# Kernel tuning notes

Measured on AMD Instinct MI355X. Metric: run time of the kernel, lower is better.

## Reference

```python
import jax, jax.numpy as jnp
import numpy as np

VOCAB, EMB, HID = 100000, 300, 600
B, S, N = 256, 64, 64
MAX_LEVEL = 3  # depth of the fixed 4-ary tree


def _tree():
    parent = np.zeros(N, np.int32)
    level = np.zeros(N, np.int32)
    for i in range(1, N):
        parent[i] = (i - 1) // 4
        level[i] = level[parent[i]] + 1
    return parent, level


def setup_inputs() -> dict:
    key = jax.random.key(0)
    ks = jax.random.split(key, 16)
    parent, level = _tree()
    E_tab = jax.random.normal(ks[0], (VOCAB, EMB), jnp.float32) * 0.1
    E_tab = E_tab.at[0].set(0.0)  # padding_idx=0
    return dict(
        premise_x=jax.random.randint(ks[1], (B, S), 0, VOCAB),
        hypothesis_x=jax.random.randint(ks[2], (B, S), 0, VOCAB),
        p_word_idx=jax.random.randint(ks[3], (B, N), -1, S),  # -1 => ones vector
        p_rel_id=jax.random.randint(ks[4], (B, N), -1, 4),    # 0..2 transformed, -1/3 identity
        h_word_idx=jax.random.randint(ks[5], (B, N), -1, S),
        h_rel_id=jax.random.randint(ks[6], (B, N), -1, 4),
        parent=jnp.asarray(parent),
        level=jnp.asarray(level),
        E_tab=E_tab,
        W_enc=jax.random.normal(ks[7], (3, EMB, EMB), jnp.float32) * 0.1,
        W0_w=jax.random.normal(ks[8], (HID, 6 * EMB), jnp.float32) * 0.1,
        W0_b=jax.random.normal(ks[9], (HID,), jnp.float32) * 0.1,
        W1_w=jax.random.normal(ks[10], (HID, HID), jnp.float32) * 0.1,
        W1_b=jax.random.normal(ks[11], (HID,), jnp.float32) * 0.1,
        W2_w=jax.random.normal(ks[12], (HID, HID), jnp.float32) * 0.1,
        W2_b=jax.random.normal(ks[13], (HID,), jnp.float32) * 0.1,
        Wout_w=jax.random.normal(ks[14], (3, HID), jnp.float32) * 0.1,
        Wout_b=jax.random.normal(ks[15], (3,), jnp.float32) * 0.1,
    )


def _encode_sg(seq, word_idx, rel_id, parent, level, W_enc):
    # Level-synchronous bottom-up evaluation of: leaf -> word,
    # internal -> relu(word * mean(rel-transformed children)).
    Bn, Nn = word_idx.shape
    Ed = seq.shape[-1]
    idx = jnp.clip(word_idx, 0, None)
    word = jnp.take_along_axis(seq, idx[:, :, None], axis=1)        # [B,N,E]
    word = jnp.where((word_idx == -1)[..., None], 1.0, word)        # word_idx==-1 => ones
    h = word
    pflat = (parent[None, :] + (jnp.arange(Bn) * Nn)[:, None]).reshape(-1)
    for l in range(MAX_LEVEL, 0, -1):
        is_child = jnp.broadcast_to(level[None, :] == l, (Bn, Nn))
        # per-relation linear W_enc[r]: h @ W.T (torch Linear, no bias)
        t_all = jnp.einsum('bne,rfe->bnrf', h, W_enc)               # [B,N,3,E]
        sel = jnp.clip(rel_id, 0, 2)[:, :, None, None]
        t = jnp.take_along_axis(t_all, sel, axis=2)[:, :, 0, :]
        t = jnp.where(((rel_id >= 0) & (rel_id <= 2))[..., None], t, h)
        contrib = jnp.where(is_child[..., None], t, 0.0).reshape(Bn * Nn, Ed)
        sums = jnp.zeros((Bn * Nn, Ed), h.dtype).at[pflat].add(contrib)
        counts = jnp.zeros((Bn * Nn,), h.dtype).at[pflat].add(
            is_child.astype(h.dtype).reshape(-1))
        mean = (sums / jnp.maximum(counts, 1.0)[:, None]).reshape(Bn, Nn, Ed)
        has_child = (counts.reshape(Bn, Nn) > 0)
        h = jnp.where(has_child[..., None], jax.nn.relu(word * mean), h)
    return h[:, 0, :]  # root representation


def reference(premise_x, hypothesis_x, p_word_idx, p_rel_id, h_word_idx, h_rel_id,
              parent, level, E_tab, W_enc, W0_w, W0_b, W1_w, W1_b, W2_w, W2_b,
              Wout_w, Wout_b):
    emb_p = E_tab[premise_x]      # [B,S,E]
    emb_h = E_tab[hypothesis_x]
    p_rep = emb_p.sum(axis=1)
    h_rep = emb_h.sum(axis=1)
    p_sg = _encode_sg(emb_p, p_word_idx, p_rel_id, parent, level, W_enc)
    h_sg = _encode_sg(emb_h, h_word_idx, h_rel_id, parent, level, W_enc)
    x = jnp.concatenate([p_rep, h_rep, p_rep - h_rep, p_rep * h_rep,
                         p_sg - h_sg, p_sg * h_sg], axis=1)  # [B,6E]
    h1 = jax.nn.relu(x @ W0_w.T + W0_b)
    h2 = jax.nn.relu(h1 @ W1_w.T + W1_b)
    h3 = jax.nn.relu(h2 @ W2_w.T + W2_b)
    return h3 @ Wout_w.T + Wout_b  # [B,3]
```

## Files before the change

### kernel.cpp

```cpp
#include <hip/hip_runtime.h>

constexpr int NB = 256;
constexpr int NS = 64;
constexpr int NN = 64;
constexpr int NE = 300;
constexpr int NH = 600;

typedef __attribute__((ext_vector_type(8))) short bf16x8;
typedef __attribute__((ext_vector_type(4))) float f32x4;

constexpr int KT0 = 57;
constexpr int KT1 = 19;
constexpr int NJT = 40;
constexpr int HP  = 640;

constexpr size_t OFF_REP = 0;
constexpr size_t SZ_REP  = (size_t)2*NB*NE;
constexpr size_t OFF_ROOT= OFF_REP + SZ_REP;
constexpr size_t OFF_WBF = OFF_ROOT + SZ_REP;
constexpr size_t SZ_WBF  = (size_t)3*20*10*64*8/2;
constexpr size_t OFF_W0S = OFF_WBF + SZ_WBF;
constexpr size_t SZ_W0S  = (size_t)KT0*NJT*64*8/2;
constexpr size_t OFF_W1S = OFF_W0S + SZ_W0S;
constexpr size_t SZ_W1S  = (size_t)KT1*NJT*64*8/2;
constexpr size_t OFF_W2S = OFF_W1S + SZ_W1S;
constexpr size_t OFF_XSW = OFF_W2S + SZ_W1S;
constexpr size_t SZ_XSW  = (size_t)KT0*16*64*8/2;
constexpr size_t OFF_H1  = OFF_XSW + SZ_XSW;
constexpr size_t SZ_H    = (size_t)NB*HP/2;
constexpr size_t OFF_H2  = OFF_H1 + SZ_H;
constexpr size_t OFF_H3  = OFF_H2 + SZ_H;

__device__ __forceinline__ ushort f2bf(float x) {
  unsigned u = __float_as_uint(x);
  unsigned r = (u + 0x7FFFu + ((u >> 16) & 1u)) >> 16;
  return (ushort)r;
}
__device__ __forceinline__ float bf2f(ushort u) {
  return __uint_as_float(((unsigned)u) << 16);
}

constexpr int NSWZ = 3*20*10*64;
constexpr int N0S  = KT0*NJT*64;
constexpr int N1S  = KT1*NJT*64;
constexpr int SETUP_ITEMS  = NSWZ + N0S + 2*N1S;
constexpr int SETUP_BLOCKS = SETUP_ITEMS/256;

__global__ __launch_bounds__(256)
void k_setup(const float* __restrict__ Wenc, const float* __restrict__ W0,
             const float* __restrict__ W1, const float* __restrict__ W2,
             ushort* __restrict__ Wbf, ushort* __restrict__ W0S,
             ushort* __restrict__ W1S, ushort* __restrict__ W2S) {
  int t = blockIdx.x*256 + threadIdx.x;
  if (t < NSWZ) {
    int lane = t & 63, rest = t >> 6;
    int ksi = rest % 10, rnt = rest / 10, nt = rnt % 20, r = rnt / 20;
    int f = nt*16 + (lane & 15), e0 = ksi*32 + (lane >> 4)*8;
    ushort v[8];
    #pragma unroll
    for (int j = 0; j < 8; j++) {
      int e = e0 + j;
      v[j] = (f < NE && e < NE) ? f2bf(Wenc[((size_t)r*NE + f)*NE + e]) : (ushort)0;
    }
    *reinterpret_cast<int4*>(&Wbf[(size_t)t*8]) = *reinterpret_cast<const int4*>(v);
    return;
  }
  t -= NSWZ;
  const float* W; ushort* D; int K;
  if (t < N0S)              { W = W0; D = W0S; K = 6*NE; }
  else { t -= N0S;
    if (t < N1S)            { W = W1; D = W1S; K = NH; }
    else { t -= N1S;          W = W2; D = W2S; K = NH; } }
  int lane = t & 63, g = t >> 6;
  int jt = g % NJT, kt = g / NJT;
  int j  = jt*16 + (lane & 15);
  int kb = kt*32 + (lane >> 4)*8;
  ushort v[8];
  #pragma unroll
  for (int i = 0; i < 8; i++) {
    int k = kb + i;
    v[i] = (j < NH && k < K) ? f2bf(W[(size_t)j*K + k]) : (ushort)0;
  }
  *reinterpret_cast<int4*>(&D[(size_t)t*8]) = *reinterpret_cast<const int4*>(v);
}

constexpr int TS = 328;

__global__ __launch_bounds__(256)
void k_tree(const int* __restrict__ px, const int* __restrict__ hx,
            const int* __restrict__ pwi, const int* __restrict__ prel,
            const int* __restrict__ hwi, const int* __restrict__ hrel,
            const float* __restrict__ Etab, const ushort* __restrict__ Wbf,
            float* __restrict__ rep, float* __restrict__ root) {
  __shared__ __align__(16) ushort hS[64*TS];
  __shared__ int xsh[64];
  __shared__ int wish[64];
  __shared__ int relsh[64];
  const int sb = blockIdx.x;
  const int s = sb >> 8, b = sb & 255;
  const int tid = threadIdx.x;

  if (tid < 64) xsh[tid] = ((s ? hx : px) + b*NS)[tid];
  else if (tid < 128) wish[tid-64] = ((s ? hwi : pwi) + b*NN)[tid-64];
  else if (tid < 192) relsh[tid-128] = ((s ? hrel : prel) + b*NN)[tid-128];
  __syncthreads();

  for (int e = tid; e < NE; e += 256) {
    float acc = 0.f;
    #pragma unroll 8
    for (int j = 0; j < NS; j++) acc += Etab[(size_t)xsh[j]*NE + e];
    rep[(size_t)sb*NE + e] = acc;
  }
  for (int flat = tid; flat < 64*75; flat += 256) {
    int n = flat / 75, c = flat % 75;
    int w = wish[n];
    float4 v;
    if (w < 0) v = float4{1.f,1.f,1.f,1.f};
    else v = *reinterpret_cast<const float4*>(&Etab[(size_t)xsh[w]*NE + c*4]);
    ushort4 o; o.x = f2bf(v.x); o.y = f2bf(v.y); o.z = f2bf(v.z); o.w = f2bf(v.w);
    *reinterpret_cast<ushort4*>(&hS[n*TS + c*4]) = o;
  }
  for (int z = tid; z < 64*10; z += 256) {
    int row = z / 10, cc = z % 10;
    *reinterpret_cast<unsigned*>(&hS[row*TS + 300 + cc*2]) = 0u;
  }
  __syncthreads();

  const int wave = tid >> 6, lane = tid & 63;
  const int mrow = lane & 15, quad = lane >> 4;

  {
    const int mb0 = 21, mb1 = 37, mb2 = 53;
    bf16x8 af[3][10];
    #pragma unroll
    for (int ks = 0; ks < 10; ks++) {
      af[0][ks] = *reinterpret_cast<const bf16x8*>(&hS[(mb0+mrow)*TS + ks*32 + quad*8]);
      af[1][ks] = *reinterpret_cast<const bf16x8*>(&hS[(mb1+mrow)*TS + ks*32 + quad*8]);
      int r2 = min(mb2+mrow, 63);
      af[2][ks] = *reinterpret_cast<const bf16x8*>(&hS[r2*TS + ks*32 + quad*8]);
    }
    __syncthreads();
    for (int pr = wave; pr < 57; pr += 4) {
      int r = pr / 19, nt = pr % 19;
      const ushort* Wb = &Wbf[(size_t)((r*20 + nt)*10)*64*8];
      f32x4 acc0 = f32x4{0.f,0.f,0.f,0.f};
      f32x4 acc1 = f32x4{0.f,0.f,0.f,0.f};
      f32x4 acc2 = f32x4{0.f,0.f,0.f,0.f};
      #pragma unroll
      for (int ks = 0; ks < 10; ks++) {
        bf16x8 bf = *reinterpret_cast<const bf16x8*>(&Wb[((size_t)ks*64 + lane)*8]);
        acc0 = __builtin_amdgcn_mfma_f32_16x16x32_bf16(af[0][ks], bf, acc0, 0, 0, 0);
        acc1 = __builtin_amdgcn_mfma_f32_16x16x32_bf16(af[1][ks], bf, acc1, 0, 0, 0);
        acc2 = __builtin_amdgcn_mfma_f32_16x16x32_bf16(af[2][ks], bf, acc2, 0, 0, 0);
      }
      int f = nt*16 + mrow;
      if (f < NE) {
        #pragma unroll
        for (int reg = 0; reg < 4; reg++) {
          int m = quad*4 + reg;
          int c0 = mb0 + m, c1 = mb1 + m, c2 = mb2 + m;
          if (relsh[c0] == r) hS[c0*TS + f] = f2bf(acc0[reg]);
          if (relsh[c1] == r) hS[c1*TS + f] = f2bf(acc1[reg]);
          if (c2 < 64 && relsh[c2] == r) hS[c2*TS + f] = f2bf(acc2[reg]);
        }
      }
    }
    __syncthreads();
    for (int f = tid; f < NE; f += 256) {
      #pragma unroll
      for (int p = 5; p <= 15; p++) {
        int nc = (p == 15) ? 3 : 4;
        float sum = 0.f;
        for (int j = 0; j < nc; j++) sum += bf2f(hS[(4*p+1+j)*TS + f]);
        float v = bf2f(hS[p*TS + f]) * sum * (1.0f/(float)nc);
        hS[p*TS + f] = f2bf(v > 0.f ? v : 0.f);
      }
    }
    __syncthreads();
  }

  {
    bf16x8 af[10];
    #pragma unroll
    for (int ks = 0; ks < 10; ks++)
      af[ks] = *reinterpret_cast<const bf16x8*>(&hS[(5+mrow)*TS + ks*32 + quad*8]);
    __syncthreads();
    for (int pr = wave; pr < 57; pr += 4) {
      int r = pr / 19, nt = pr % 19;
      const ushort* Wb = &Wbf[(size_t)((r*20 + nt)*10)*64*8];
      f32x4 acc = f32x4{0.f,0.f,0.f,0.f};
      #pragma unroll
      for (int ks = 0; ks < 10; ks++) {
        bf16x8 bf = *reinterpret_cast<const bf16x8*>(&Wb[((size_t)ks*64 + lane)*8]);
        acc = __builtin_amdgcn_mfma_f32_16x16x32_bf16(af[ks], bf, acc, 0, 0, 0);
      }
      int f = nt*16 + mrow;
      if (f < NE) {
        #pragma unroll
        for (int reg = 0; reg < 4; reg++) {
          int c = 5 + quad*4 + reg;
          if (relsh[c] == r) hS[c*TS + f] = f2bf(acc[reg]);
        }
      }
    }
    __syncthreads();
    for (int f = tid; f < NE; f += 256) {
      #pragma unroll
      for (int p = 1; p <= 4; p++) {
        float sum = 0.f;
        #pragma unroll
        for (int j = 0; j < 4; j++) sum += bf2f(hS[(4*p+1+j)*TS + f]);
        float v = bf2f(hS[p*TS + f]) * sum * 0.25f;
        hS[p*TS + f] = f2bf(v > 0.f ? v : 0.f);
      }
    }
    __syncthreads();
  }

  {
    bool rp0 = (relsh[1]==0)|(relsh[2]==0)|(relsh[3]==0)|(relsh[4]==0);
    bool rp1 = (relsh[1]==1)|(relsh[2]==1)|(relsh[3]==1)|(relsh[4]==1);
    bool rp2 = (relsh[1]==2)|(relsh[2]==2)|(relsh[3]==2)|(relsh[4]==2);
    bf16x8 af[10];
    #pragma unroll
    for (int ks = 0; ks < 10; ks++)
      af[ks] = *reinterpret_cast<const bf16x8*>(&hS[(1+min(mrow,3))*TS + ks*32 + quad*8]);
    __syncthreads();
    for (int pr = wave; pr < 57; pr += 4) {
      int r = pr / 19, nt = pr % 19;
      if ((r==0 && !rp0) || (r==1 && !rp1) || (r==2 && !rp2)) continue;
      const ushort* Wb = &Wbf[(size_t)((r*20 + nt)*10)*64*8];
      f32x4 acc = f32x4{0.f,0.f,0.f,0.f};
      #pragma unroll
      for (int ks = 0; ks < 10; ks++) {
        bf16x8 bf = *reinterpret_cast<const bf16x8*>(&Wb[((size_t)ks*64 + lane)*8]);
        acc = __builtin_amdgcn_mfma_f32_16x16x32_bf16(af[ks], bf, acc, 0, 0, 0);
      }
      int f = nt*16 + mrow;
      if (f < NE) {
        #pragma unroll
        for (int reg = 0; reg < 4; reg++) {
          int m = quad*4 + reg;
          if (m < 4 && relsh[1+m] == r) hS[(1+m)*TS + f] = f2bf(acc[reg]);
        }
      }
    }
    __syncthreads();
    for (int f = tid; f < NE; f += 256) {
      float sum = 0.f;
      #pragma unroll
      for (int c = 1; c <= 4; c++) sum += bf2f(hS[c*TS + f]);
      float v = bf2f(hS[0*TS + f]) * sum * 0.25f;
      root[(size_t)sb*NE + f] = v > 0.f ? v : 0.f;
    }
  }
}

constexpr int FEAT_ITEMS  = KT0*16*64;
constexpr int FEAT_BLOCKS = FEAT_ITEMS/256;

__global__ __launch_bounds__(256)
void k_feat(const float* __restrict__ rep, const float* __restrict__ root,
            ushort* __restrict__ Xsw) {
  int t = blockIdx.x*256 + threadIdx.x;
  int lane = t & 63, g = t >> 6;
  int mt = g % 16, kt = g / 16;
  int b  = mt*16 + (lane & 15);
  int kb = kt*32 + (lane >> 4)*8;
  const float* rp = rep  + (size_t)b*NE;
  const float* rh = rep  + (size_t)(NB+b)*NE;
  const float* tp = root + (size_t)b*NE;
  const float* th = root + (size_t)(NB+b)*NE;
  ushort v[8];
  #pragma unroll
  for (int i = 0; i < 8; i++) {
    int k = kb + i;
    float x = 0.f;
    if (k < 6*NE) {
      int seg = k / NE, e = k - seg*NE;
      switch (seg) {
        case 0:  x = rp[e]; break;
        case 1:  x = rh[e]; break;
        case 2:  x = rp[e] - rh[e]; break;
        case 3:  x = rp[e] * rh[e]; break;
        case 4:  x = tp[e] - th[e]; break;
        default: x = tp[e] * th[e]; break;
      }
    }
    v[i] = f2bf(x);
  }
  *reinterpret_cast<int4*>(&Xsw[(size_t)t*8]) = *reinterpret_cast<const int4*>(v);
}

__device__ __forceinline__ void fc_epi(f32x4 acc, int row, int j,
                                       const float* __restrict__ bias,
                                       ushort* __restrict__ hout) {
  float bj = (j < NH) ? bias[j] : 0.f;
  #pragma unroll
  for (int r = 0; r < 4; r++) {
    float v = acc[r] + bj;
    v = v > 0.f ? v : 0.f;
    if (j < 608) hout[(size_t)(row + r)*HP + j] = f2bf(v);
  }
}

__global__ __launch_bounds__(256)
void k_gemm(const ushort* __restrict__ A, const ushort* __restrict__ Wsw,
            const float* __restrict__ bias, ushort* __restrict__ hout,
            int nstep, int mode) {
  const int tid = threadIdx.x;
  const int wv = tid >> 6, lane = tid & 63;
  const int bx = blockIdx.x, by = blockIdx.y;
  const int b0 = bx*64, j0 = by*64;

  const ushort* ap;
  size_t astride;
  if (mode == 0) {
    ap = A + ((size_t)((size_t)bx*4 + wv)*64 + lane)*8;
    astride = (size_t)16*64*8;
  } else {
    ap = A + (size_t)(b0 + wv*16 + (lane & 15))*HP + (lane >> 4)*8;
    astride = 32;
  }
  const ushort* wp = Wsw + ((size_t)(by*4)*64 + lane)*8;
  constexpr size_t WSTRIDE = (size_t)NJT*64*8;

  f32x4 acc0{0.f,0.f,0.f,0.f}, acc1{0.f,0.f,0.f,0.f};
  f32x4 acc2{0.f,0.f,0.f,0.f}, acc3{0.f,0.f,0.f,0.f};
  for (int t = 0; t < nstep; t++) {
    bf16x8 a  = *reinterpret_cast<const bf16x8*>(ap);
    bf16x8 w0 = *reinterpret_cast<const bf16x8*>(wp);
    bf16x8 w1 = *reinterpret_cast<const bf16x8*>(wp + 512);
    bf16x8 w2 = *reinterpret_cast<const bf16x8*>(wp + 1024);
    bf16x8 w3 = *reinterpret_cast<const bf16x8*>(wp + 1536);
    acc0 = __builtin_amdgcn_mfma_f32_16x16x32_bf16(a, w0, acc0, 0, 0, 0);
    acc1 = __builtin_amdgcn_mfma_f32_16x16x32_bf16(a, w1, acc1, 0, 0, 0);
    acc2 = __builtin_amdgcn_mfma_f32_16x16x32_bf16(a, w2, acc2, 0, 0, 0);
    acc3 = __builtin_amdgcn_mfma_f32_16x16x32_bf16(a, w3, acc3, 0, 0, 0);
    ap += astride;
    wp += WSTRIDE;
  }
  int row = b0 + wv*16 + (lane >> 4)*4;
  int jb  = j0 + (lane & 15);
  fc_epi(acc0, row, jb +  0, bias, hout);
  fc_epi(acc1, row, jb + 16, bias, hout);
  fc_epi(acc2, row, jb + 32, bias, hout);
  fc_epi(acc3, row, jb + 48, bias, hout);
}

__global__ __launch_bounds__(64)
void k_out(const ushort* __restrict__ h3, const float* __restrict__ Wout,
           const float* __restrict__ bout, float* __restrict__ out) {
  int b = blockIdx.x, tid = threadIdx.x;
  float a0 = 0.f, a1 = 0.f, a2 = 0.f;
  for (int k = tid; k < NH; k += 64) {
    float xv = bf2f(h3[(size_t)b*HP + k]);
    a0 += xv * Wout[k];
    a1 += xv * Wout[NH + k];
    a2 += xv * Wout[2*NH + k];
  }
  #pragma unroll
  for (int off = 32; off > 0; off >>= 1) {
    a0 += __shfl_down(a0, off, 64);
    a1 += __shfl_down(a1, off, 64);
    a2 += __shfl_down(a2, off, 64);
  }
  if (tid == 0) {
    out[b*3 + 0] = a0 + bout[0];
    out[b*3 + 1] = a1 + bout[1];
    out[b*3 + 2] = a2 + bout[2];
  }
}

extern "C" void kernel_launch(void* const* d_in, const int* in_sizes, int n_in,
                              void* d_out, int out_size, void* d_ws, size_t ws_size,
                              hipStream_t stream) {
  const int*   px    = (const int*)d_in[0];
  const int*   hx    = (const int*)d_in[1];
  const int*   pwi   = (const int*)d_in[2];
  const int*   prel  = (const int*)d_in[3];
  const int*   hwi   = (const int*)d_in[4];
  const int*   hrel  = (const int*)d_in[5];
  const float* Etab  = (const float*)d_in[8];
  const float* Wenc  = (const float*)d_in[9];
  const float* W0w   = (const float*)d_in[10];
  const float* W0b   = (const float*)d_in[11];
  const float* W1w   = (const float*)d_in[12];
  const float* W1b   = (const float*)d_in[13];
  const float* W2w   = (const float*)d_in[14];
  const float* W2b   = (const float*)d_in[15];
  const float* Woutw = (const float*)d_in[16];
  const float* Woutb = (const float*)d_in[17];

  float* ws   = (float*)d_ws;
  float*  rep  = ws + OFF_REP;
  float*  root = ws + OFF_ROOT;
  ushort* Wbf  = (ushort*)(ws + OFF_WBF);
  ushort* W0S  = (ushort*)(ws + OFF_W0S);
  ushort* W1S  = (ushort*)(ws + OFF_W1S);
  ushort* W2S  = (ushort*)(ws + OFF_W2S);
  ushort* Xsw  = (ushort*)(ws + OFF_XSW);
  ushort* h1   = (ushort*)(ws + OFF_H1);
  ushort* h2   = (ushort*)(ws + OFF_H2);
  ushort* h3   = (ushort*)(ws + OFF_H3);
  float* outp = (float*)d_out;

  dim3 blk(256);
  k_setup<<<dim3(SETUP_BLOCKS), blk, 0, stream>>>(
      Wenc, W0w, W1w, W2w, Wbf, W0S, W1S, W2S);
  k_tree<<<dim3(2*NB), blk, 0, stream>>>(
      px, hx, pwi, prel, hwi, hrel, Etab, Wbf, rep, root);
  k_feat<<<dim3(FEAT_BLOCKS), blk, 0, stream>>>(rep, root, Xsw);
  k_gemm<<<dim3(4,10), blk, 0, stream>>>(Xsw, W0S, W0b, h1, KT0, 0);
  k_gemm<<<dim3(4,10), blk, 0, stream>>>(h1,  W1S, W1b, h2, KT1, 1);
  k_gemm<<<dim3(4,10), blk, 0, stream>>>(h2,  W2S, W2b, h3, KT1, 1);
  k_out<<<dim3(NB), dim3(64), 0, stream>>>(h3, Woutw, Woutb, outp);
}
```

Baseline: 314.2 us.

## Fuse all stages into one persistent kernel with grid barriers and split-K FC

Replaces the seven separate launches (weight swizzle, tree encoder, feature build, three FC GEMMs, output) with one persistent 512-block kernel synchronised by an atomic-counter grid barrier. The FC layers now use 160 blocks, with each wave taking a K-slice and partial sums reduced through shared memory, instead of 40 blocks. The aim is to remove launch gaps and raise parallelism in the small GEMMs. The risks are spin-barrier cost and a deadlock if not all blocks are co-resident.

```diff
diff --git a/kernel.cpp b/kernel.cpp
--- a/kernel.cpp
+++ b/kernel.cpp
@@ -5,6 +5,7 @@
 constexpr int NN = 64;
 constexpr int NE = 300;
 constexpr int NH = 600;
+constexpr int NBLK = 512;
 
 typedef __attribute__((ext_vector_type(8))) short bf16x8;
 typedef __attribute__((ext_vector_type(4))) float f32x4;
@@ -30,6 +31,7 @@
 constexpr size_t SZ_H    = (size_t)NB*HP/2;
 constexpr size_t OFF_H2  = OFF_H1 + SZ_H;
 constexpr size_t OFF_H3  = OFF_H2 + SZ_H;
+constexpr size_t OFF_CNT = OFF_H3 + SZ_H;
 
 __device__ __forceinline__ ushort f2bf(float x) {
   unsigned u = __float_as_uint(x);
@@ -40,294 +42,51 @@
   return __uint_as_float(((unsigned)u) << 16);
 }
 
+__device__ __forceinline__ void gridbar(unsigned* cnt, unsigned target) {
+  __syncthreads();
+  if (threadIdx.x == 0) {
+    __threadfence();
+    atomicAdd(cnt, 1u);
+    while (atomicAdd(cnt, 0u) < target) __builtin_amdgcn_s_sleep(2);
+    __threadfence();
+  }
+  __syncthreads();
+}
+
 constexpr int NSWZ = 3*20*10*64;
 constexpr int N0S  = KT0*NJT*64;
 constexpr int N1S  = KT1*NJT*64;
-constexpr int SETUP_ITEMS  = NSWZ + N0S + 2*N1S;
-constexpr int SETUP_BLOCKS = SETUP_ITEMS/256;
-
-__global__ __launch_bounds__(256)
-void k_setup(const float* __restrict__ Wenc, const float* __restrict__ W0,
-             const float* __restrict__ W1, const float* __restrict__ W2,
-             ushort* __restrict__ Wbf, ushort* __restrict__ W0S,
-             ushort* __restrict__ W1S, ushort* __restrict__ W2S) {
-  int t = blockIdx.x*256 + threadIdx.x;
-  if (t < NSWZ) {
-    int lane = t & 63, rest = t >> 6;
-    int ksi = rest % 10, rnt = rest / 10, nt = rnt % 20, r = rnt / 20;
-    int f = nt*16 + (lane & 15), e0 = ksi*32 + (lane >> 4)*8;
-    ushort v[8];
-    #pragma unroll
-    for (int j = 0; j < 8; j++) {
-      int e = e0 + j;
-      v[j] = (f < NE && e < NE) ? f2bf(Wenc[((size_t)r*NE + f)*NE + e]) : (ushort)0;
-    }
-    *reinterpret_cast<int4*>(&Wbf[(size_t)t*8]) = *reinterpret_cast<const int4*>(v);
-    return;
-  }
-  t -= NSWZ;
-  const float* W; ushort* D; int K;
-  if (t < N0S)              { W = W0; D = W0S; K = 6*NE; }
-  else { t -= N0S;
-    if (t < N1S)            { W = W1; D = W1S; K = NH; }
-    else { t -= N1S;          W = W2; D = W2S; K = NH; } }
-  int lane = t & 63, g = t >> 6;
-  int jt = g % NJT, kt = g / NJT;
-  int j  = jt*16 + (lane & 15);
-  int kb = kt*32 + (lane >> 4)*8;
-  ushort v[8];
-  #pragma unroll
-  for (int i = 0; i < 8; i++) {
-    int k = kb + i;
-    v[i] = (j < NH && k < K) ? f2bf(W[(size_t)j*K + k]) : (ushort)0;
-  }
-  *reinterpret_cast<int4*>(&D[(size_t)t*8]) = *reinterpret_cast<const int4*>(v);
-}
+constexpr int SETUP_ITEMS = NSWZ + N0S + 2*N1S;
+constexpr int FEAT_ITEMS  = KT0*16*64;
 
 constexpr int TS = 328;
 
-__global__ __launch_bounds__(256)
-void k_tree(const int* __restrict__ px, const int* __restrict__ hx,
-            const int* __restrict__ pwi, const int* __restrict__ prel,
-            const int* __restrict__ hwi, const int* __restrict__ hrel,
-            const float* __restrict__ Etab, const ushort* __restrict__ Wbf,
-            float* __restrict__ rep, float* __restrict__ root) {
-  __shared__ __align__(16) ushort hS[64*TS];
-  __shared__ int xsh[64];
-  __shared__ int wish[64];
-  __shared__ int relsh[64];
-  const int sb = blockIdx.x;
-  const int s = sb >> 8, b = sb & 255;
-  const int tid = threadIdx.x;
-
-  if (tid < 64) xsh[tid] = ((s ? hx : px) + b*NS)[tid];
-  else if (tid < 128) wish[tid-64] = ((s ? hwi : pwi) + b*NN)[tid-64];
-  else if (tid < 192) relsh[tid-128] = ((s ? hrel : prel) + b*NN)[tid-128];
-  __syncthreads();
-
-  for (int e = tid; e < NE; e += 256) {
-    float acc = 0.f;
-    #pragma unroll 8
-    for (int j = 0; j < NS; j++) acc += Etab[(size_t)xsh[j]*NE + e];
-    rep[(size_t)sb*NE + e] = acc;
-  }
-  for (int flat = tid; flat < 64*75; flat += 256) {
-    int n = flat / 75, c = flat % 75;
-    int w = wish[n];
-    float4 v;
-    if (w < 0) v = float4{1.f,1.f,1.f,1.f};
-    else v = *reinterpret_cast<const float4*>(&Etab[(size_t)xsh[w]*NE + c*4]);
-    ushort4 o; o.x = f2bf(v.x); o.y = f2bf(v.y); o.z = f2bf(v.z); o.w = f2bf(v.w);
-    *reinterpret_cast<ushort4*>(&hS[n*TS + c*4]) = o;
-  }
-  for (int z = tid; z < 64*10; z += 256) {
-    int row = z / 10, cc = z % 10;
-    *reinterpret_cast<unsigned*>(&hS[row*TS + 300 + cc*2]) = 0u;
-  }
-  __syncthreads();
-
-  const int wave = tid >> 6, lane = tid & 63;
-  const int mrow = lane & 15, quad = lane >> 4;
-
-  {
-    const int mb0 = 21, mb1 = 37, mb2 = 53;
-    bf16x8 af[3][10];
-    #pragma unroll
-    for (int ks = 0; ks < 10; ks++) {
-      af[0][ks] = *reinterpret_cast<const bf16x8*>(&hS[(mb0+mrow)*TS + ks*32 + quad*8]);
-      af[1][ks] = *reinterpret_cast<const bf16x8*>(&hS[(mb1+mrow)*TS + ks*32 + quad*8]);
-      int r2 = min(mb2+mrow, 63);
-      af[2][ks] = *reinterpret_cast<const bf16x8*>(&hS[r2*TS + ks*32 + quad*8]);
-    }
-    __syncthreads();
-    for (int pr = wave; pr < 57; pr += 4) {
-      int r = pr / 19, nt = pr % 19;
-      const ushort* Wb = &Wbf[(size_t)((r*20 + nt)*10)*64*8];
-      f32x4 acc0 = f32x4{0.f,0.f,0.f,0.f};
-      f32x4 acc1 = f32x4{0.f,0.f,0.f,0.f};
-      f32x4 acc2 = f32x4{0.f,0.f,0.f,0.f};
-      #pragma unroll
-      for (int ks = 0; ks < 10; ks++) {
-        bf16x8 bf = *reinterpret_cast<const bf16x8*>(&Wb[((size_t)ks*64 + lane)*8]);
-        acc0 = __builtin_amdgcn_mfma_f32_16x16x32_bf16(af[0][ks], bf, acc0, 0, 0, 0);
-        acc1 = __builtin_amdgcn_mfma_f32_16x16x32_bf16(af[1][ks], bf, acc1, 0, 0, 0);
-        acc2 = __builtin_amdgcn_mfma_f32_16x16x32_bf16(af[2][ks], bf, acc2, 0, 0, 0);
-      }
-      int f = nt*16 + mrow;
-      if (f < NE) {
-        #pragma unroll
-        for (int reg = 0; reg < 4; reg++) {
-          int m = quad*4 + reg;
-          int c0 = mb0 + m, c1 = mb1 + m, c2 = mb2 + m;
-          if (relsh[c0] == r) hS[c0*TS + f] = f2bf(acc0[reg]);
-          if (relsh[c1] == r) hS[c1*TS + f] = f2bf(acc1[reg]);
-          if (c2 < 64 && relsh[c2] == r) hS[c2*TS + f] = f2bf(acc2[reg]);
-        }
-      }
-    }
-    __syncthreads();
-    for (int f = tid; f < NE; f += 256) {
-      #pragma unroll
-      for (int p = 5; p <= 15; p++) {
-        int nc = (p == 15) ? 3 : 4;
-        float sum = 0.f;
-        for (int j = 0; j < nc; j++) sum += bf2f(hS[(4*p+1+j)*TS + f]);
-        float v = bf2f(hS[p*TS + f]) * sum * (1.0f/(float)nc);
-        hS[p*TS + f] = f2bf(v > 0.f ? v : 0.f);
-      }
-    }
-    __syncthreads();
-  }
-
-  {
-    bf16x8 af[10];
-    #pragma unroll
-    for (int ks = 0; ks < 10; ks++)
-      af[ks] = *reinterpret_cast<const bf16x8*>(&hS[(5+mrow)*TS + ks*32 + quad*8]);
-    __syncthreads();
-    for (int pr = wave; pr < 57; pr += 4) {
-      int r = pr / 19, nt = pr % 19;
-      const ushort* Wb = &Wbf[(size_t)((r*20 + nt)*10)*64*8];
-      f32x4 acc = f32x4{0.f,0.f,0.f,0.f};
-      #pragma unroll
-      for (int ks = 0; ks < 10; ks++) {
-        bf16x8 bf = *reinterpret_cast<const bf16x8*>(&Wb[((size_t)ks*64 + lane)*8]);
-        acc = __builtin_amdgcn_mfma_f32_16x16x32_bf16(af[ks], bf, acc, 0, 0, 0);
-      }
-      int f = nt*16 + mrow;
-      if (f < NE) {
-        #pragma unroll
-        for (int reg = 0; reg < 4; reg++) {
-          int c = 5 + quad*4 + reg;
-          if (relsh[c] == r) hS[c*TS + f] = f2bf(acc[reg]);
-        }
-      }
-    }
-    __syncthreads();
-    for (int f = tid; f < NE; f += 256) {
-      #pragma unroll
-      for (int p = 1; p <= 4; p++) {
-        float sum = 0.f;
-        #pragma unroll
-        for (int j = 0; j < 4; j++) sum += bf2f(hS[(4*p+1+j)*TS + f]);
-        float v = bf2f(hS[p*TS + f]) * sum * 0.25f;
-        hS[p*TS + f] = f2bf(v > 0.f ? v : 0.f);
-      }
-    }
-    __syncthreads();
-  }
-
-  {
-    bool rp0 = (relsh[1]==0)|(relsh[2]==0)|(relsh[3]==0)|(relsh[4]==0);
-    bool rp1 = (relsh[1]==1)|(relsh[2]==1)|(relsh[3]==1)|(relsh[4]==1);
-    bool rp2 = (relsh[1]==2)|(relsh[2]==2)|(relsh[3]==2)|(relsh[4]==2);
-    bf16x8 af[10];
-    #pragma unroll
-    for (int ks = 0; ks < 10; ks++)
-      af[ks] = *reinterpret_cast<const bf16x8*>(&hS[(1+min(mrow,3))*TS + ks*32 + quad*8]);
-    __syncthreads();
-    for (int pr = wave; pr < 57; pr += 4) {
-      int r = pr / 19, nt = pr % 19;
-      if ((r==0 && !rp0) || (r==1 && !rp1) || (r==2 && !rp2)) continue;
-      const ushort* Wb = &Wbf[(size_t)((r*20 + nt)*10)*64*8];
-      f32x4 acc = f32x4{0.f,0.f,0.f,0.f};
-      #pragma unroll
-      for (int ks = 0; ks < 10; ks++) {
-        bf16x8 bf = *reinterpret_cast<const bf16x8*>(&Wb[((size_t)ks*64 + lane)*8]);
-        acc = __builtin_amdgcn_mfma_f32_16x16x32_bf16(af[ks], bf, acc, 0, 0, 0);
-      }
-      int f = nt*16 + mrow;
-      if (f < NE) {
-        #pragma unroll
-        for (int reg = 0; reg < 4; reg++) {
-          int m = quad*4 + reg;
-          if (m < 4 && relsh[1+m] == r) hS[(1+m)*TS + f] = f2bf(acc[reg]);
-        }
-      }
-    }
-    __syncthreads();
-    for (int f = tid; f < NE; f += 256) {
-      float sum = 0.f;
-      #pragma unroll
-      for (int c = 1; c <= 4; c++) sum += bf2f(hS[c*TS + f]);
-      float v = bf2f(hS[0*TS + f]) * sum * 0.25f;
-      root[(size_t)sb*NE + f] = v > 0.f ? v : 0.f;
-    }
-  }
-}
-
-constexpr int FEAT_ITEMS  = KT0*16*64;
-constexpr int FEAT_BLOCKS = FEAT_ITEMS/256;
-
-__global__ __launch_bounds__(256)
-void k_feat(const float* __restrict__ rep, const float* __restrict__ root,
-            ushort* __restrict__ Xsw) {
-  int t = blockIdx.x*256 + threadIdx.x;
-  int lane = t & 63, g = t >> 6;
-  int mt = g % 16, kt = g / 16;
-  int b  = mt*16 + (lane & 15);
-  int kb = kt*32 + (lane >> 4)*8;
-  const float* rp = rep  + (size_t)b*NE;
-  const float* rh = rep  + (size_t)(NB+b)*NE;
-  const float* tp = root + (size_t)b*NE;
-  const float* th = root + (size_t)(NB+b)*NE;
-  ushort v[8];
-  #pragma unroll
-  for (int i = 0; i < 8; i++) {
-    int k = kb + i;
-    float x = 0.f;
-    if (k < 6*NE) {
-      int seg = k / NE, e = k - seg*NE;
-      switch (seg) {
-        case 0:  x = rp[e]; break;
-        case 1:  x = rh[e]; break;
-        case 2:  x = rp[e] - rh[e]; break;
-        case 3:  x = rp[e] * rh[e]; break;
-        case 4:  x = tp[e] - th[e]; break;
-        default: x = tp[e] * th[e]; break;
-      }
-    }
-    v[i] = f2bf(x);
-  }
-  *reinterpret_cast<int4*>(&Xsw[(size_t)t*8]) = *reinterpret_cast<const int4*>(v);
-}
-
-__device__ __forceinline__ void fc_epi(f32x4 acc, int row, int j,
-                                       const float* __restrict__ bias,
-                                       ushort* __restrict__ hout) {
-  float bj = (j < NH) ? bias[j] : 0.f;
-  #pragma unroll
-  for (int r = 0; r < 4; r++) {
-    float v = acc[r] + bj;
-    v = v > 0.f ? v : 0.f;
-    if (j < 608) hout[(size_t)(row + r)*HP + j] = f2bf(v);
-  }
-}
-
-__global__ __launch_bounds__(256)
-void k_gemm(const ushort* __restrict__ A, const ushort* __restrict__ Wsw,
-            const float* __restrict__ bias, ushort* __restrict__ hout,
-            int nstep, int mode) {
-  const int tid = threadIdx.x;
-  const int wv = tid >> 6, lane = tid & 63;
-  const int bx = blockIdx.x, by = blockIdx.y;
-  const int b0 = bx*64, j0 = by*64;
+__device__ void fc_layer(const ushort* __restrict__ Arm,
+                         const ushort* __restrict__ Xs,
+                         const ushort* __restrict__ Wsw,
+                         const float* __restrict__ bias,
+                         ushort* __restrict__ hout,
+                         int nkt, float* red) {
+  const int blk = blockIdx.x;
+  if (blk >= 160) return;
+  const int tid = threadIdx.x, wv = tid >> 6, lane = tid & 63;
+  const int bx = blk / 10, by = blk % 10;
 
   const ushort* ap;
-  size_t astride;
-  if (mode == 0) {
-    ap = A + ((size_t)((size_t)bx*4 + wv)*64 + lane)*8;
-    astride = (size_t)16*64*8;
+  size_t ast;
+  if (Xs) {
+    ap  = Xs + (((size_t)wv*16 + bx)*64 + lane)*8;
+    ast = (size_t)4*16*64*8;
   } else {
-    ap = A + (size_t)(b0 + wv*16 + (lane & 15))*HP + (lane >> 4)*8;
-    astride = 32;
-  }
-  const ushort* wp = Wsw + ((size_t)(by*4)*64 + lane)*8;
-  constexpr size_t WSTRIDE = (size_t)NJT*64*8;
+    ap  = Arm + ((size_t)(bx*16 + (lane & 15)))*HP + ((lane >> 4)*8) + (size_t)wv*32;
+    ast = (size_t)4*32;
+  }
+  const ushort* wp = Wsw + (((size_t)wv*NJT + (size_t)by*4)*64 + lane)*8;
+  const size_t wst = (size_t)4*NJT*64*8;
 
   f32x4 acc0{0.f,0.f,0.f,0.f}, acc1{0.f,0.f,0.f,0.f};
   f32x4 acc2{0.f,0.f,0.f,0.f}, acc3{0.f,0.f,0.f,0.f};
-  for (int t = 0; t < nstep; t++) {
+  for (int t = wv; t < nkt; t += 4) {
     bf16x8 a  = *reinterpret_cast<const bf16x8*>(ap);
     bf16x8 w0 = *reinterpret_cast<const bf16x8*>(wp);
     bf16x8 w1 = *reinterpret_cast<const bf16x8*>(wp + 512);
@@ -337,38 +96,312 @@
     acc1 = __builtin_amdgcn_mfma_f32_16x16x32_bf16(a, w1, acc1, 0, 0, 0);
     acc2 = __builtin_amdgcn_mfma_f32_16x16x32_bf16(a, w2, acc2, 0, 0, 0);
     acc3 = __builtin_amdgcn_mfma_f32_16x16x32_bf16(a, w3, acc3, 0, 0, 0);
-    ap += astride;
-    wp += WSTRIDE;
-  }
-  int row = b0 + wv*16 + (lane >> 4)*4;
-  int jb  = j0 + (lane & 15);
-  fc_epi(acc0, row, jb +  0, bias, hout);
-  fc_epi(acc1, row, jb + 16, bias, hout);
-  fc_epi(acc2, row, jb + 32, bias, hout);
-  fc_epi(acc3, row, jb + 48, bias, hout);
-}
-
-__global__ __launch_bounds__(64)
-void k_out(const ushort* __restrict__ h3, const float* __restrict__ Wout,
-           const float* __restrict__ bout, float* __restrict__ out) {
-  int b = blockIdx.x, tid = threadIdx.x;
-  float a0 = 0.f, a1 = 0.f, a2 = 0.f;
-  for (int k = tid; k < NH; k += 64) {
-    float xv = bf2f(h3[(size_t)b*HP + k]);
-    a0 += xv * Wout[k];
-    a1 += xv * Wout[NH + k];
-    a2 += xv * Wout[2*NH + k];
-  }
+    ap += ast; wp += wst;
+  }
+  *reinterpret_cast<f32x4*>(&red[(((size_t)0*4 + wv)*64 + lane)*4]) = acc0;
+  *reinterpret_cast<f32x4*>(&red[(((size_t)1*4 + wv)*64 + lane)*4]) = acc1;
+  *reinterpret_cast<f32x4*>(&red[(((size_t)2*4 + wv)*64 + lane)*4]) = acc2;
+  *reinterpret_cast<f32x4*>(&red[(((size_t)3*4 + wv)*64 + lane)*4]) = acc3;
+  __syncthreads();
+  f32x4 s{0.f,0.f,0.f,0.f};
   #pragma unroll
-  for (int off = 32; off > 0; off >>= 1) {
-    a0 += __shfl_down(a0, off, 64);
-    a1 += __shfl_down(a1, off, 64);
-    a2 += __shfl_down(a2, off, 64);
-  }
-  if (tid == 0) {
-    out[b*3 + 0] = a0 + bout[0];
-    out[b*3 + 1] = a1 + bout[1];
-    out[b*3 + 2] = a2 + bout[2];
+  for (int w = 0; w < 4; w++) {
+    f32x4 p = *reinterpret_cast<f32x4*>(&red[(((size_t)wv*4 + w)*64 + lane)*4]);
+    s[0] += p[0]; s[1] += p[1]; s[2] += p[2]; s[3] += p[3];
+  }
+  int row0 = bx*16 + (lane >> 4)*4;
+  int j = by*64 + wv*16 + (lane & 15);
+  float bj = (j < NH) ? bias[j] : 0.f;
+  #pragma unroll
+  for (int r = 0; r < 4; r++) {
+    float v = s[r] + bj;
+    v = v > 0.f ? v : 0.f;
+    if (j < 608) hout[(size_t)(row0 + r)*HP + j] = f2bf(v);
+  }
+}
+
+__global__ __launch_bounds__(256, 4)
+void k_all(const int* __restrict__ px, const int* __restrict__ hx,
+           const int* __restrict__ pwi, const int* __restrict__ prel,
+           const int* __restrict__ hwi, const int* __restrict__ hrel,
+           const float* __restrict__ Etab, const float* __restrict__ Wenc,
+           const float* __restrict__ W0w, const float* __restrict__ W0b,
+           const float* __restrict__ W1w, const float* __restrict__ W1b,
+           const float* __restrict__ W2w, const float* __restrict__ W2b,
+           const float* __restrict__ Woutw, const float* __restrict__ Woutb,
+           float* __restrict__ rep, float* __restrict__ root,
+           ushort* __restrict__ Wbf, ushort* __restrict__ W0S,
+           ushort* __restrict__ W1S, ushort* __restrict__ W2S,
+           ushort* __restrict__ Xsw, ushort* __restrict__ h1,
+           ushort* __restrict__ h2, ushort* __restrict__ h3,
+           unsigned* cnt, float* __restrict__ outp) {
+  __shared__ __align__(16) ushort hS[64*TS];
+  __shared__ int xsh[64];
+  __shared__ int wish[64];
+  __shared__ int relsh[64];
+  const int tid = threadIdx.x;
+  unsigned bar = 0;
+
+  for (int t0 = blockIdx.x*256 + tid; t0 < SETUP_ITEMS; t0 += NBLK*256) {
+    int t = t0;
+    if (t < NSWZ) {
+      int lane = t & 63, rest = t >> 6;
+      int ksi = rest % 10, rnt = rest / 10, nt = rnt % 20, r = rnt / 20;
+      int f = nt*16 + (lane & 15), e0 = ksi*32 + (lane >> 4)*8;
+      ushort v[8];
+      #pragma unroll
+      for (int j = 0; j < 8; j++) {
+        int e = e0 + j;
+        v[j] = (f < NE && e < NE) ? f2bf(Wenc[((size_t)r*NE + f)*NE + e]) : (ushort)0;
+      }
+      *reinterpret_cast<int4*>(&Wbf[(size_t)t*8]) = *reinterpret_cast<const int4*>(v);
+    } else {
+      t -= NSWZ;
+      const float* W; ushort* D; int K;
+      if (t < N0S)            { W = W0w; D = W0S; K = 6*NE; }
+      else { t -= N0S;
+        if (t < N1S)          { W = W1w; D = W1S; K = NH; }
+        else { t -= N1S;        W = W2w; D = W2S; K = NH; } }
+      int lane = t & 63, g = t >> 6;
+      int jt = g % NJT, kt = g / NJT;
+      int j  = jt*16 + (lane & 15);
+      int kb = kt*32 + (lane >> 4)*8;
+      ushort v[8];
+      #pragma unroll
+      for (int i = 0; i < 8; i++) {
+        int k = kb + i;
+        v[i] = (j < NH && k < K) ? f2bf(W[(size_t)j*K + k]) : (ushort)0;
+      }
+      *reinterpret_cast<int4*>(&D[(size_t)t*8]) = *reinterpret_cast<const int4*>(v);
+    }
+  }
+  bar += NBLK; gridbar(cnt, bar);
+
+  {
+    const int sb = blockIdx.x;
+    const int s = sb >> 8, b = sb & 255;
+
+    if (tid < 64) xsh[tid] = ((s ? hx : px) + b*NS)[tid];
+    else if (tid < 128) wish[tid-64] = ((s ? hwi : pwi) + b*NN)[tid-64];
+    else if (tid < 192) relsh[tid-128] = ((s ? hrel : prel) + b*NN)[tid-128];
+    __syncthreads();
+
+    for (int e = tid; e < NE; e += 256) {
+      float acc = 0.f;
+      #pragma unroll 8
+      for (int j = 0; j < NS; j++) acc += Etab[(size_t)xsh[j]*NE + e];
+      rep[(size_t)sb*NE + e] = acc;
+    }
+    for (int flat = tid; flat < 64*75; flat += 256) {
+      int n = flat / 75, c = flat % 75;
+      int w = wish[n];
+      float4 v;
+      if (w < 0) v = float4{1.f,1.f,1.f,1.f};
+      else v = *reinterpret_cast<const float4*>(&Etab[(size_t)xsh[w]*NE + c*4]);
+      ushort4 o; o.x = f2bf(v.x); o.y = f2bf(v.y); o.z = f2bf(v.z); o.w = f2bf(v.w);
+      *reinterpret_cast<ushort4*>(&hS[n*TS + c*4]) = o;
+    }
+    for (int z = tid; z < 64*10; z += 256) {
+      int row = z / 10, cc = z % 10;
+      *reinterpret_cast<unsigned*>(&hS[row*TS + 300 + cc*2]) = 0u;
+    }
+    __syncthreads();
+
+    const int wave = tid >> 6, lane = tid & 63;
+    const int mrow = lane & 15, quad = lane >> 4;
+
+    {
+      const int mb0 = 21, mb1 = 37, mb2 = 53;
+      bf16x8 af[3][10];
+      #pragma unroll
+      for (int ks = 0; ks < 10; ks++) {
+        af[0][ks] = *reinterpret_cast<const bf16x8*>(&hS[(mb0+mrow)*TS + ks*32 + quad*8]);
+        af[1][ks] = *reinterpret_cast<const bf16x8*>(&hS[(mb1+mrow)*TS + ks*32 + quad*8]);
+        int r2 = min(mb2+mrow, 63);
+        af[2][ks] = *reinterpret_cast<const bf16x8*>(&hS[r2*TS + ks*32 + quad*8]);
+      }
+      __syncthreads();
+      for (int pr = wave; pr < 57; pr += 4) {
+        int r = pr / 19, nt = pr % 19;
+        const ushort* Wb = &Wbf[(size_t)((r*20 + nt)*10)*64*8];
+        f32x4 acc0 = f32x4{0.f,0.f,0.f,0.f};
+        f32x4 acc1 = f32x4{0.f,0.f,0.f,0.f};
+        f32x4 acc2 = f32x4{0.f,0.f,0.f,0.f};
+        #pragma unroll
+        for (int ks = 0; ks < 10; ks++) {
+          bf16x8 bf = *reinterpret_cast<const bf16x8*>(&Wb[((size_t)ks*64 + lane)*8]);
+          acc0 = __builtin_amdgcn_mfma_f32_16x16x32_bf16(af[0][ks], bf, acc0, 0, 0, 0);
+          acc1 = __builtin_amdgcn_mfma_f32_16x16x32_bf16(af[1][ks], bf, acc1, 0, 0, 0);
+          acc2 = __builtin_amdgcn_mfma_f32_16x16x32_bf16(af[2][ks], bf, acc2, 0, 0, 0);
+        }
+        int f = nt*16 + mrow;
+        if (f < NE) {
+          #pragma unroll
+          for (int reg = 0; reg < 4; reg++) {
+            int m = quad*4 + reg;
+            int c0 = mb0 + m, c1 = mb1 + m, c2 = mb2 + m;
+            if (relsh[c0] == r) hS[c0*TS + f] = f2bf(acc0[reg]);
+            if (relsh[c1] == r) hS[c1*TS + f] = f2bf(acc1[reg]);
+            if (c2 < 64 && relsh[c2] == r) hS[c2*TS + f] = f2bf(acc2[reg]);
+          }
+        }
+      }
+      __syncthreads();
+      for (int f = tid; f < NE; f += 256) {
+        #pragma unroll
+        for (int p = 5; p <= 15; p++) {
+          int nc = (p == 15) ? 3 : 4;
+          float sum = 0.f;
+          for (int j = 0; j < nc; j++) sum += bf2f(hS[(4*p+1+j)*TS + f]);
+          float v = bf2f(hS[p*TS + f]) * sum * (1.0f/(float)nc);
+          hS[p*TS + f] = f2bf(v > 0.f ? v : 0.f);
+        }
+      }
+      __syncthreads();
+    }
+    {
+      bf16x8 af[10];
+      #pragma unroll
+      for (int ks = 0; ks < 10; ks++)
+        af[ks] = *reinterpret_cast<const bf16x8*>(&hS[(5+mrow)*TS + ks*32 + quad*8]);
+      __syncthreads();
+      for (int pr = wave; pr < 57; pr += 4) {
+        int r = pr / 19, nt = pr % 19;
+        const ushort* Wb = &Wbf[(size_t)((r*20 + nt)*10)*64*8];
+        f32x4 acc = f32x4{0.f,0.f,0.f,0.f};
+        #pragma unroll
+        for (int ks = 0; ks < 10; ks++) {
+          bf16x8 bf = *reinterpret_cast<const bf16x8*>(&Wb[((size_t)ks*64 + lane)*8]);
+          acc = __builtin_amdgcn_mfma_f32_16x16x32_bf16(af[ks], bf, acc, 0, 0, 0);
+        }
+        int f = nt*16 + mrow;
+        if (f < NE) {
+          #pragma unroll
+          for (int reg = 0; reg < 4; reg++) {
+            int c = 5 + quad*4 + reg;
+            if (relsh[c] == r) hS[c*TS + f] = f2bf(acc[reg]);
+          }
+        }
+      }
+      __syncthreads();
+      for (int f = tid; f < NE; f += 256) {
+        #pragma unroll
+        for (int p = 1; p <= 4; p++) {
+          float sum = 0.f;
+          #pragma unroll
+          for (int j = 0; j < 4; j++) sum += bf2f(hS[(4*p+1+j)*TS + f]);
+          float v = bf2f(hS[p*TS + f]) * sum * 0.25f;
+          hS[p*TS + f] = f2bf(v > 0.f ? v : 0.f);
+        }
+      }
+      __syncthreads();
+    }
+    {
+      bool rp0 = (relsh[1]==0)|(relsh[2]==0)|(relsh[3]==0)|(relsh[4]==0);
+      bool rp1 = (relsh[1]==1)|(relsh[2]==1)|(relsh[3]==1)|(relsh[4]==1);
+      bool rp2 = (relsh[1]==2)|(relsh[2]==2)|(relsh[3]==2)|(relsh[4]==2);
+      bf16x8 af[10];
+      #pragma unroll
+      for (int ks = 0; ks < 10; ks++)
+        af[ks] = *reinterpret_cast<const bf16x8*>(&hS[(1+min(mrow,3))*TS + ks*32 + quad*8]);
+      __syncthreads();
+      for (int pr = wave; pr < 57; pr += 4) {
+        int r = pr / 19, nt = pr % 19;
+        if ((r==0 && !rp0) || (r==1 && !rp1) || (r==2 && !rp2)) continue;
+        const ushort* Wb = &Wbf[(size_t)((r*20 + nt)*10)*64*8];
+        f32x4 acc = f32x4{0.f,0.f,0.f,0.f};
+        #pragma unroll
+        for (int ks = 0; ks < 10; ks++) {
+          bf16x8 bf = *reinterpret_cast<const bf16x8*>(&Wb[((size_t)ks*64 + lane)*8]);
+          acc = __builtin_amdgcn_mfma_f32_16x16x32_bf16(af[ks], bf, acc, 0, 0, 0);
+        }
+        int f = nt*16 + mrow;
+        if (f < NE) {
+          #pragma unroll
+          for (int reg = 0; reg < 4; reg++) {
+            int m = quad*4 + reg;
+            if (m < 4 && relsh[1+m] == r) hS[(1+m)*TS + f] = f2bf(acc[reg]);
+          }
+        }
+      }
+      __syncthreads();
+      for (int f = tid; f < NE; f += 256) {
+        float sum = 0.f;
+        #pragma unroll
+        for (int c = 1; c <= 4; c++) sum += bf2f(hS[c*TS + f]);
+        float v = bf2f(hS[0*TS + f]) * sum * 0.25f;
+        root[(size_t)sb*NE + f] = v > 0.f ? v : 0.f;
+      }
+    }
+  }
+  bar += NBLK; gridbar(cnt, bar);
+
+  {
+    int t = blockIdx.x*256 + tid;
+    if (t < FEAT_ITEMS) {
+      int lane = t & 63, g = t >> 6;
+      int mt = g % 16, kt = g / 16;
+      int b  = mt*16 + (lane & 15);
+      int kb = kt*32 + (lane >> 4)*8;
+      const float* rp = rep  + (size_t)b*NE;
+      const float* rh = rep  + (size_t)(NB+b)*NE;
+      const float* tp = root + (size_t)b*NE;
+      const float* th = root + (size_t)(NB+b)*NE;
+      ushort v[8];
+      #pragma unroll
+      for (int i = 0; i < 8; i++) {
+        int k = kb + i;
+        float x = 0.f;
+        if (k < 6*NE) {
+          int seg = k / NE, e = k - seg*NE;
+          switch (seg) {
+            case 0:  x = rp[e]; break;
+            case 1:  x = rh[e]; break;
+            case 2:  x = rp[e] - rh[e]; break;
+            case 3:  x = rp[e] * rh[e]; break;
+            case 4:  x = tp[e] - th[e]; break;
+            default: x = tp[e] * th[e]; break;
+          }
+        }
+        v[i] = f2bf(x);
+      }
+      *reinterpret_cast<int4*>(&Xsw[(size_t)t*8]) = *reinterpret_cast<const int4*>(v);
+    }
+  }
+  bar += NBLK; gridbar(cnt, bar);
+
+  float* red = reinterpret_cast<float*>(hS);
+  for (int l = 0; l < 3; l++) {
+    const ushort* Arm = (l == 0) ? nullptr : (l == 1 ? h1 : h2);
+    const ushort* Xs  = (l == 0) ? Xsw : nullptr;
+    const ushort* Wsw = (l == 0) ? W0S : (l == 1 ? W1S : W2S);
+    const float*  bia = (l == 0) ? W0b : (l == 1 ? W1b : W2b);
+    ushort*       ho  = (l == 0) ? h1  : (l == 1 ? h2  : h3);
+    int nkt = (l == 0) ? KT0 : KT1;
+    fc_layer(Arm, Xs, Wsw, bia, ho, nkt, red);
+    bar += NBLK; gridbar(cnt, bar);
+  }
+
+  if (blockIdx.x < NB && tid < 64) {
+    int b = blockIdx.x;
+    float a0 = 0.f, a1 = 0.f, a2 = 0.f;
+    for (int k = tid; k < NH; k += 64) {
+      float xv = bf2f(h3[(size_t)b*HP + k]);
+      a0 += xv * Woutw[k];
+      a1 += xv * Woutw[NH + k];
+      a2 += xv * Woutw[2*NH + k];
+    }
+    #pragma unroll
+    for (int off = 32; off > 0; off >>= 1) {
+      a0 += __shfl_down(a0, off, 64);
+      a1 += __shfl_down(a1, off, 64);
+      a2 += __shfl_down(a2, off, 64);
+    }
+    if (tid == 0) {
+      outp[b*3 + 0] = a0 + Woutb[0];
+      outp[b*3 + 1] = a1 + Woutb[1];
+      outp[b*3 + 2] = a2 + Woutb[2];
+    }
   }
 }
 
@@ -403,16 +436,12 @@
   ushort* h1   = (ushort*)(ws + OFF_H1);
   ushort* h2   = (ushort*)(ws + OFF_H2);
   ushort* h3   = (ushort*)(ws + OFF_H3);
+  unsigned* cnt = (unsigned*)(ws + OFF_CNT);
   float* outp = (float*)d_out;
 
-  dim3 blk(256);
-  k_setup<<<dim3(SETUP_BLOCKS), blk, 0, stream>>>(
-      Wenc, W0w, W1w, W2w, Wbf, W0S, W1S, W2S);
-  k_tree<<<dim3(2*NB), blk, 0, stream>>>(
-      px, hx, pwi, prel, hwi, hrel, Etab, Wbf, rep, root);
-  k_feat<<<dim3(FEAT_BLOCKS), blk, 0, stream>>>(rep, root, Xsw);
-  k_gemm<<<dim3(4,10), blk, 0, stream>>>(Xsw, W0S, W0b, h1, KT0, 0);
-  k_gemm<<<dim3(4,10), blk, 0, stream>>>(h1,  W1S, W1b, h2, KT1, 1);
-  k_gemm<<<dim3(4,10), blk, 0, stream>>>(h2,  W2S, W2b, h3, KT1, 1);
-  k_out<<<dim3(NB), dim3(64), 0, stream>>>(h3, Woutw, Woutb, outp);
-}
+  hipMemsetAsync(cnt, 0, sizeof(unsigned), stream);
+  k_all<<<dim3(NBLK), dim3(256), 0, stream>>>(
+      px, hx, pwi, prel, hwi, hrel, Etab, Wenc,
+      W0w, W0b, W1w, W1b, W2w, W2b, Woutw, Woutb,
+      rep, root, Wbf, W0S, W1S, W2S, Xsw, h1, h2, h3, cnt, outp);
+}
```

Measured after the change: 613.6 us. 1.95x slower.
